# Optimization experiments

Measured on AMD Instinct MI355X. Metric: run time of the kernel, lower is better.

The kernel has to match this reference:

```python
import jax, jax.numpy as jnp
import numpy as np

B, N, F = 4, 3000, 128

def setup_inputs() -> dict:
    key = jax.random.key(0)
    k1, k2, k3, k4 = jax.random.split(key, 4)
    x = jax.random.normal(k1, (B, N, F), dtype=jnp.float32)
    adj = jax.random.uniform(k2, (B, N, N), dtype=jnp.float32)
    h0 = jax.random.normal(k3, (B, N, F), dtype=jnp.float32)
    stdv = 1.0 / np.sqrt(F)
    theta = jax.random.uniform(k4, (F, F), dtype=jnp.float32, minval=-stdv, maxval=stdv)
    return {
        "x": x, "adj": adj, "h0": h0, "theta": theta,
        "lamda": jnp.float32(0.5), "alpha": jnp.float32(0.1), "l": 4,
    }

def _normalize_adj(adj):
    # add self loops, then D^{-1/2} A D^{-1/2} via elementwise row/col scaling
    # (same math as diag-embed + inverse + two bmms in the original)
    n = adj.shape[1]
    adj = adj + jnp.eye(n, dtype=adj.dtype)
    deg = jnp.sum(adj, axis=2)                      # [B, N]
    d_inv_sqrt = jax.lax.rsqrt(deg)                 # [B, N]
    return d_inv_sqrt[:, :, None] * adj * d_inv_sqrt[:, None, :]

def reference(x, adj, h0, theta, lamda, alpha, l):
    adj_n = _normalize_adj(adj)
    beta = jnp.log(lamda / l + 1.0)
    hi = jnp.einsum('bnm,bmf->bnf', adj_n, x)       # aggregation
    support = (1.0 - alpha) * hi + alpha * h0       # variant=False path
    r = support
    out = beta * jnp.einsum('bnf,fg->bng', support, theta) + (1.0 - beta) * r
    return out
```

## Files before the change

kernel.cpp:

```cpp
#include <hip/hip_runtime.h>
#include <hip/hip_bf16.h>
#include <math.h>

#define BB 4
#define NN 3000
#define NR 3008
#define NC 3072
#define FF 128
#define NKC 96
#define NIT 188

typedef __bf16 bf16x8 __attribute__((ext_vector_type(8)));
typedef __bf16 bf16x4 __attribute__((ext_vector_type(4)));
typedef __bf16 bf16x8a __attribute__((ext_vector_type(8), aligned(8)));
typedef __bf16 bf16x4a __attribute__((ext_vector_type(4), aligned(4)));
typedef float  f32x4  __attribute__((ext_vector_type(4)));

__global__ __launch_bounds__(256) void k_degpk2(const float* __restrict__ adj,
                                                float* __restrict__ dis,
                                                __bf16* __restrict__ apk) {
    int wid  = (blockIdx.x * 256 + threadIdx.x) >> 6;
    int lane = threadIdx.x & 63;
    if (wid >= BB * NN) return;
    int b = wid / NN, i = wid - b * NN;
    const float4* row4 = (const float4*)(adj + (size_t)wid * NN);
    __bf16* prow = apk + ((size_t)b * NR + i) * NC;
    float s = 0.f;
    for (int c = lane; c < 768; c += 64) {
        float4 v = {0.f, 0.f, 0.f, 0.f};
        if (c < 750) v = row4[c];
        s += (v.x + v.y) + (v.z + v.w);
        bf16x4a o;
        o[0] = (__bf16)v.x; o[1] = (__bf16)v.y;
        o[2] = (__bf16)v.z; o[3] = (__bf16)v.w;
        *(bf16x4a*)(prow + c * 4) = o;
    }
    for (int off = 32; off > 0; off >>= 1) s += __shfl_down(s, off, 64);
    if (lane == 0) dis[wid] = 1.0f / sqrtf(s + 1.0f);
}

__global__ __launch_bounds__(256) void k_xpk(const float* __restrict__ x,
                                             const float* __restrict__ dis,
                                             const float* __restrict__ theta,
                                             __bf16* __restrict__ xpk,
                                             __bf16* __restrict__ thpk) {
    int b  = blockIdx.y, kc = blockIdx.x;
    int t  = threadIdx.x, w = t >> 6, l = t & 63;
    int m  = l & 15, q = l >> 4;
    #pragma unroll
    for (int h = 0; h < 2; ++h) {
        int nt = w + h * 4;
        int f  = nt * 16 + m;
        bf16x8 v;
        #pragma unroll
        for (int j = 0; j < 8; ++j) {
            int k = kc * 32 + q * 8 + j;
            float val = 0.f;
            if (k < NN) val = dis[b * NN + k] * x[((size_t)b * NN + k) * FF + f];
            v[j] = (__bf16)val;
        }
        *(bf16x8*)(xpk + ((size_t)(b * 8 + nt) * NKC + kc) * 512 + l * 8) = v;
    }
    if (b == 0 && kc < 4) {
        #pragma unroll
        for (int h = 0; h < 2; ++h) {
            int nt = w + h * 4;
            bf16x8 v;
            #pragma unroll
            for (int j = 0; j < 8; ++j) {
                int k = kc * 32 + q * 8 + j;
                v[j] = (__bf16)theta[k * FF + nt * 16 + m];
            }
            *(bf16x8*)(thpk + ((size_t)(nt * 4 + kc)) * 512 + l * 8) = v;
        }
    }
}

__global__ __launch_bounds__(256) void k_aggs2(const __bf16* __restrict__ apk,
                                               const __bf16* __restrict__ xpk,
                                               const __bf16* __restrict__ thpk,
                                               const float* __restrict__ x,
                                               const float* __restrict__ h0,
                                               const float* __restrict__ dis,
                                               float* __restrict__ out,
                                               const float* __restrict__ alpha_p,
                                               const float* __restrict__ lamda_p,
                                               const int* __restrict__ l_p) {
    __shared__ __bf16 stile[16][140];
    const int id = blockIdx.x;
    const int b  = (id >> 1) & 3;
    const int it = (id >> 3) * 2 + (id & 1);
    const int i0 = it * 16;
    const int t  = threadIdx.x, w = t >> 6, l = t & 63;
    const int m  = l & 15, quad = l >> 4;
    const int n0 = w * 32;
    const __bf16* A0 = apk + ((size_t)b * NR + (i0 + m)) * NC + quad * 8;
    const __bf16* B0 = xpk + ((size_t)(b * 8 + 2 * w) * NKC) * 512 + l * 8;
    const __bf16* B1 = B0 + (size_t)NKC * 512;
    f32x4 acc0 = {0.f, 0.f, 0.f, 0.f};
    f32x4 acc1 = {0.f, 0.f, 0.f, 0.f};

    #pragma unroll 8
    for (int kc = 0; kc < NKC; ++kc) {
        bf16x8 a  = *(const bf16x8*)(A0 + kc * 32);
        bf16x8 b0 = *(const bf16x8*)(B0 + (size_t)kc * 512);
        bf16x8 b1 = *(const bf16x8*)(B1 + (size_t)kc * 512);
        acc0 = __builtin_amdgcn_mfma_f32_16x16x32_bf16(a, b0, acc0, 0, 0, 0);
        acc1 = __builtin_amdgcn_mfma_f32_16x16x32_bf16(a, b1, acc1, 0, 0, 0);
    }

    const float alpha = *alpha_p;
    const float beta  = logf(*lamda_p / (float)(*l_p) + 1.0f);
    float s0v[4], s1v[4];
    #pragma unroll
    for (int r = 0; r < 4; ++r) {
        int row  = quad * 4 + r;
        int irow = i0 + row;
        float s0 = 0.f, s1 = 0.f;
        if (irow < NN) {
            float  di   = dis[b * NN + irow];
            size_t base = ((size_t)b * NN + irow) * FF;
            int c0 = n0 + m, c1 = n0 + 16 + m;
            s0 = (1.f - alpha) * (di * acc0[r] + di * di * x[base + c0]) + alpha * h0[base + c0];
            s1 = (1.f - alpha) * (di * acc1[r] + di * di * x[base + c1]) + alpha * h0[base + c1];
        }
        s0v[r] = s0; s1v[r] = s1;
        stile[row][n0 + m]      = (__bf16)s0;
        stile[row][n0 + 16 + m] = (__bf16)s1;
    }
    __syncthreads();
    f32x4 o0 = {0.f, 0.f, 0.f, 0.f};
    f32x4 o1 = {0.f, 0.f, 0.f, 0.f};
    const __bf16* T0 = thpk + (size_t)(2 * w * 4) * 512 + l * 8;
    const __bf16* T1 = T0 + 4 * 512;
    #pragma unroll
    for (int kc = 0; kc < 4; ++kc) {
        bf16x4a alo = *(const bf16x4a*)&stile[m][kc * 32 + quad * 8];
        bf16x4a ahi = *(const bf16x4a*)&stile[m][kc * 32 + quad * 8 + 4];
        bf16x8 a = __builtin_shufflevector(alo, ahi, 0, 1, 2, 3, 4, 5, 6, 7);
        bf16x8 tb0 = *(const bf16x8*)(T0 + (size_t)kc * 512);
        bf16x8 tb1 = *(const bf16x8*)(T1 + (size_t)kc * 512);
        o0 = __builtin_amdgcn_mfma_f32_16x16x32_bf16(a, tb0, o0, 0, 0, 0);
        o1 = __builtin_amdgcn_mfma_f32_16x16x32_bf16(a, tb1, o1, 0, 0, 0);
    }
    const float omb = 1.f - beta;
    #pragma unroll
    for (int r = 0; r < 4; ++r) {
        int irow = i0 + quad * 4 + r;
        if (irow < NN) {
            size_t base = ((size_t)b * NN + irow) * FF;
            out[base + n0 + m]      = beta * o0[r] + omb * s0v[r];
            out[base + n0 + 16 + m] = beta * o1[r] + omb * s1v[r];
        }
    }
}

#define TS 532
__global__ __launch_bounds__(256) void k_deg(const float* __restrict__ adj,
                                             float* __restrict__ dis) {
    int wid  = (blockIdx.x * 256 + threadIdx.x) >> 6;
    int lane = threadIdx.x & 63;
    if (wid >= BB * NN) return;
    const float4* row = (const float4*)(adj + (size_t)wid * NN);
    float s = 0.f;
    for (int c = lane; c < NN / 4; c += 64) {
        float4 v = row[c];
        s += (v.x + v.y) + (v.z + v.w);
    }
    for (int off = 32; off > 0; off >>= 1) s += __shfl_down(s, off, 64);
    if (lane == 0) dis[wid] = 1.0f / sqrtf(s + 1.0f);
}

__global__ __launch_bounds__(256) void k_agg(const float* __restrict__ adj,
                                             const __bf16* __restrict__ xpk,
                                             const __bf16* __restrict__ thpk,
                                             const float* __restrict__ x,
                                             const float* __restrict__ h0,
                                             const float* __restrict__ dis,
                                             float* __restrict__ out,
                                             const float* __restrict__ alpha_p,
                                             const float* __restrict__ lamda_p,
                                             const int* __restrict__ l_p) {
    __shared__ __bf16 tile[2][16][TS];
    __shared__ __bf16 stile[16][140];
    const int id = blockIdx.x;
    const int b  = (id >> 1) & 3;
    const int it = (id >> 3) * 2 + (id & 1);
    const int i0 = it * 16;
    const int t  = threadIdx.x, w = t >> 6, l = t & 63;
    const int m  = l & 15, quad = l >> 4;
    const int n0 = w * 32;
    const __bf16* B0 = xpk + ((size_t)(b * 8 + 2 * w) * NKC) * 512 + l * 8;
    const __bf16* B1 = B0 + (size_t)NKC * 512;
    f32x4 acc0 = {0.f, 0.f, 0.f, 0.f};
    f32x4 acc1 = {0.f, 0.f, 0.f, 0.f};

    float4 pu[4], pv[4];
    auto load_chunk = [&](int c) {
        #pragma unroll
        for (int i = 0; i < 4; ++i) {
            int row  = i * 4 + w;
            int irow = i0 + row;
            int col  = c * 512 + l * 8;
            float4 u = {0.f, 0.f, 0.f, 0.f}, v = {0.f, 0.f, 0.f, 0.f};
            if (irow < NN && col < NN) {
                const float* p = adj + ((size_t)b * NN + irow) * NN + col;
                u = *(const float4*)p;
                v = *(const float4*)(p + 4);
            }
            pu[i] = u; pv[i] = v;
        }
    };
    auto store_chunk = [&](int cb) {
        #pragma unroll
        for (int i = 0; i < 4; ++i) {
            int row = i * 4 + w;
            bf16x8a s;
            s[0] = (__bf16)pu[i].x; s[1] = (__bf16)pu[i].y;
            s[2] = (__bf16)pu[i].z; s[3] = (__bf16)pu[i].w;
            s[4] = (__bf16)pv[i].x; s[5] = (__bf16)pv[i].y;
            s[6] = (__bf16)pv[i].z; s[7] = (__bf16)pv[i].w;
            *(bf16x8a*)&tile[cb][row][l * 8] = s;
        }
    };

    load_chunk(0);
    store_chunk(0);
    __syncthreads();
    for (int c = 0; c < 6; ++c) {
        int cb = c & 1;
        if (c < 5) load_chunk(c + 1);
        #pragma unroll 4
        for (int kcl = 0; kcl < 16; ++kcl) {
            int kc = c * 16 + kcl;
            bf16x8 a = *(const bf16x8a*)&tile[cb][m][kcl * 32 + quad * 8];
            bf16x8 b0 = *(const bf16x8*)(B0 + (size_t)kc * 512);
            bf16x8 b1 = *(const bf16x8*)(B1 + (size_t)kc * 512);
            acc0 = __builtin_amdgcn_mfma_f32_16x16x32_bf16(a, b0, acc0, 0, 0, 0);
            acc1 = __builtin_amdgcn_mfma_f32_16x16x32_bf16(a, b1, acc1, 0, 0, 0);
        }
        if (c < 5) store_chunk(cb ^ 1);
        __syncthreads();
    }

    const float alpha = *alpha_p;
    const float beta  = logf(*lamda_p / (float)(*l_p) + 1.0f);
    float s0v[4], s1v[4];
    #pragma unroll
    for (int r = 0; r < 4; ++r) {
        int row  = quad * 4 + r;
        int irow = i0 + row;
        float s0 = 0.f, s1 = 0.f;
        if (irow < NN) {
            float  di   = dis[b * NN + irow];
            size_t base = ((size_t)b * NN + irow) * FF;
            int c0 = n0 + m, c1 = n0 + 16 + m;
            s0 = (1.f - alpha) * (di * acc0[r] + di * di * x[base + c0]) + alpha * h0[base + c0];
            s1 = (1.f - alpha) * (di * acc1[r] + di * di * x[base + c1]) + alpha * h0[base + c1];
        }
        s0v[r] = s0; s1v[r] = s1;
        stile[row][n0 + m]      = (__bf16)s0;
        stile[row][n0 + 16 + m] = (__bf16)s1;
    }
    __syncthreads();
    f32x4 o0 = {0.f, 0.f, 0.f, 0.f};
    f32x4 o1 = {0.f, 0.f, 0.f, 0.f};
    const __bf16* T0 = thpk + (size_t)(2 * w * 4) * 512 + l * 8;
    const __bf16* T1 = T0 + 4 * 512;
    #pragma unroll
    for (int kc = 0; kc < 4; ++kc) {
        bf16x4a alo = *(const bf16x4a*)&stile[m][kc * 32 + quad * 8];
        bf16x4a ahi = *(const bf16x4a*)&stile[m][kc * 32 + quad * 8 + 4];
        bf16x8 a = __builtin_shufflevector(alo, ahi, 0, 1, 2, 3, 4, 5, 6, 7);
        bf16x8 tb0 = *(const bf16x8*)(T0 + (size_t)kc * 512);
        bf16x8 tb1 = *(const bf16x8*)(T1 + (size_t)kc * 512);
        o0 = __builtin_amdgcn_mfma_f32_16x16x32_bf16(a, tb0, o0, 0, 0, 0);
        o1 = __builtin_amdgcn_mfma_f32_16x16x32_bf16(a, tb1, o1, 0, 0, 0);
    }
    const float omb = 1.f - beta;
    #pragma unroll
    for (int r = 0; r < 4; ++r) {
        int irow = i0 + quad * 4 + r;
        if (irow < NN) {
            size_t base = ((size_t)b * NN + irow) * FF;
            out[base + n0 + m]      = beta * o0[r] + omb * s0v[r];
            out[base + n0 + 16 + m] = beta * o1[r] + omb * s1v[r];
        }
    }
}

__global__ __launch_bounds__(256) void k_thpk_fb(const float* __restrict__ theta,
                                                 __bf16* __restrict__ thpk) {
    int kc = blockIdx.x;
    int t  = threadIdx.x, w = t >> 6, l = t & 63;
    int m  = l & 15, q = l >> 4;
    #pragma unroll
    for (int h = 0; h < 2; ++h) {
        int nt = w + h * 4;
        bf16x8 v;
        #pragma unroll
        for (int j = 0; j < 8; ++j) {
            int k = kc * 32 + q * 8 + j;
            v[j] = (__bf16)theta[k * FF + nt * 16 + m];
        }
        *(bf16x8*)(thpk + ((size_t)(nt * 4 + kc)) * 512 + l * 8) = v;
    }
}

__global__ __launch_bounds__(256) void k_xpk_fb(const float* __restrict__ x,
                                                const float* __restrict__ dis,
                                                __bf16* __restrict__ xpk) {
    int b  = blockIdx.y, kc = blockIdx.x;
    int t  = threadIdx.x, w = t >> 6, l = t & 63;
    int m  = l & 15, q = l >> 4;
    #pragma unroll
    for (int h = 0; h < 2; ++h) {
        int nt = w + h * 4;
        int f  = nt * 16 + m;
        bf16x8 v;
        #pragma unroll
        for (int j = 0; j < 8; ++j) {
            int k = kc * 32 + q * 8 + j;
            float val = 0.f;
            if (k < NN) val = dis[b * NN + k] * x[((size_t)b * NN + k) * FF + f];
            v[j] = (__bf16)val;
        }
        *(bf16x8*)(xpk + ((size_t)(b * 8 + nt) * NKC + kc) * 512 + l * 8) = v;
    }
}


extern "C" void kernel_launch(void* const* d_in, const int* in_sizes, int n_in,
                              void* d_out, int out_size, void* d_ws, size_t ws_size,
                              hipStream_t stream) {
    const float* x      = (const float*)d_in[0];
    const float* adj    = (const float*)d_in[1];
    const float* h0     = (const float*)d_in[2];
    const float* theta  = (const float*)d_in[3];
    const float* lamda  = (const float*)d_in[4];
    const float* alpha  = (const float*)d_in[5];
    const int*   l      = (const int*)d_in[6];
    float* out = (float*)d_out;

    char* ws = (char*)d_ws;

    const size_t APK_OFF = 3276800;
    const size_t WS_NEED = APK_OFF + (size_t)BB * NR * NC * 2;

    if (ws_size >= WS_NEED) {
        float*  dis  = (float*)ws;
        __bf16* thpk = (__bf16*)(ws + 65536);
        __bf16* xpk  = (__bf16*)(ws + 131072);
        __bf16* apk  = (__bf16*)(ws + APK_OFF);

        k_degpk2<<<dim3((BB * NN) / 4), 256, 0, stream>>>(adj, dis, apk);
        k_xpk<<<dim3(NKC, BB), 256, 0, stream>>>(x, dis, theta, xpk, thpk);
        k_aggs2<<<dim3(NIT * BB), 256, 0, stream>>>(apk, xpk, thpk, x, h0, dis, out,
                                                    alpha, lamda, l);
    } else {
        float*  dis  = (float*)ws;
        __bf16* xpk  = (__bf16*)(ws + 65536);
        __bf16* thpk = (__bf16*)(ws + 3276800);

        k_deg<<<dim3((BB * NN) / 4), 256, 0, stream>>>(adj, dis);
        k_thpk_fb<<<dim3(4), 256, 0, stream>>>(theta, thpk);
        k_xpk_fb<<<dim3(NKC, BB), 256, 0, stream>>>(x, dis, xpk);
        k_agg<<<dim3(NIT * BB), 256, 0, stream>>>(adj, xpk, thpk, x, h0, dis, out,
                                                  alpha, lamda, l);
    }
}
```

Measured before the change: 305.6 us.

## Stage packed adjacency rows through double-buffered LDS in aggregation kernel

The aggregation kernel now loads 512-column chunks of the packed bf16 adjacency with coalesced row-wide loads into a double-buffered shared tile. It prefetches the next chunk into registers while MFMAs consume the current one. Previously each lane read strided 16-byte pieces directly from global memory. The packing kernel also now covers the padding rows (NR instead of NN) and writes zeros there, so the padded tile rows are defined. The cost is extra LDS traffic, more shared memory per block and a barrier per chunk.

```diff
diff --git a/kernel.cpp b/kernel.cpp
--- a/kernel.cpp
+++ b/kernel.cpp
@@ -9,6 +9,7 @@
 #define FF 128
 #define NKC 96
 #define NIT 188
+#define TS  532
 
 typedef __bf16 bf16x8 __attribute__((ext_vector_type(8)));
 typedef __bf16 bf16x4 __attribute__((ext_vector_type(4)));
@@ -21,14 +22,15 @@
                                                 __bf16* __restrict__ apk) {
     int wid  = (blockIdx.x * 256 + threadIdx.x) >> 6;
     int lane = threadIdx.x & 63;
-    if (wid >= BB * NN) return;
-    int b = wid / NN, i = wid - b * NN;
-    const float4* row4 = (const float4*)(adj + (size_t)wid * NN);
+    if (wid >= BB * NR) return;
+    int b = wid / NR, i = wid - b * NR;
+    const bool rowv = i < NN;
+    const float4* row4 = (const float4*)(adj + ((size_t)b * NN + i) * NN);
     __bf16* prow = apk + ((size_t)b * NR + i) * NC;
     float s = 0.f;
     for (int c = lane; c < 768; c += 64) {
         float4 v = {0.f, 0.f, 0.f, 0.f};
-        if (c < 750) v = row4[c];
+        if (rowv && c < 750) v = row4[c];
         s += (v.x + v.y) + (v.z + v.w);
         bf16x4a o;
         o[0] = (__bf16)v.x; o[1] = (__bf16)v.y;
@@ -36,7 +38,7 @@
         *(bf16x4a*)(prow + c * 4) = o;
     }
     for (int off = 32; off > 0; off >>= 1) s += __shfl_down(s, off, 64);
-    if (lane == 0) dis[wid] = 1.0f / sqrtf(s + 1.0f);
+    if (lane == 0 && rowv) dis[b * NN + i] = 1.0f / sqrtf(s + 1.0f);
 }
 
 __global__ __launch_bounds__(256) void k_xpk(const float* __restrict__ x,
@@ -76,16 +78,17 @@
     }
 }
 
-__global__ __launch_bounds__(256) void k_aggs2(const __bf16* __restrict__ apk,
-                                               const __bf16* __restrict__ xpk,
-                                               const __bf16* __restrict__ thpk,
-                                               const float* __restrict__ x,
-                                               const float* __restrict__ h0,
-                                               const float* __restrict__ dis,
-                                               float* __restrict__ out,
-                                               const float* __restrict__ alpha_p,
-                                               const float* __restrict__ lamda_p,
-                                               const int* __restrict__ l_p) {
+__global__ __launch_bounds__(256) void k_agg3(const __bf16* __restrict__ apk,
+                                              const __bf16* __restrict__ xpk,
+                                              const __bf16* __restrict__ thpk,
+                                              const float* __restrict__ x,
+                                              const float* __restrict__ h0,
+                                              const float* __restrict__ dis,
+                                              float* __restrict__ out,
+                                              const float* __restrict__ alpha_p,
+                                              const float* __restrict__ lamda_p,
+                                              const int* __restrict__ l_p) {
+    __shared__ __bf16 tile[2][16][TS];
     __shared__ __bf16 stile[16][140];
     const int id = blockIdx.x;
     const int b  = (id >> 1) & 3;
@@ -94,19 +97,45 @@
     const int t  = threadIdx.x, w = t >> 6, l = t & 63;
     const int m  = l & 15, quad = l >> 4;
     const int n0 = w * 32;
-    const __bf16* A0 = apk + ((size_t)b * NR + (i0 + m)) * NC + quad * 8;
+    const __bf16* Abase = apk + ((size_t)b * NR + i0) * NC;
     const __bf16* B0 = xpk + ((size_t)(b * 8 + 2 * w) * NKC) * 512 + l * 8;
     const __bf16* B1 = B0 + (size_t)NKC * 512;
     f32x4 acc0 = {0.f, 0.f, 0.f, 0.f};
     f32x4 acc1 = {0.f, 0.f, 0.f, 0.f};
 
-    #pragma unroll 8
-    for (int kc = 0; kc < NKC; ++kc) {
-        bf16x8 a  = *(const bf16x8*)(A0 + kc * 32);
-        bf16x8 b0 = *(const bf16x8*)(B0 + (size_t)kc * 512);
-        bf16x8 b1 = *(const bf16x8*)(B1 + (size_t)kc * 512);
-        acc0 = __builtin_amdgcn_mfma_f32_16x16x32_bf16(a, b0, acc0, 0, 0, 0);
-        acc1 = __builtin_amdgcn_mfma_f32_16x16x32_bf16(a, b1, acc1, 0, 0, 0);
+    bf16x8a st[4];
+    auto load_chunk = [&](int c) {
+        #pragma unroll
+        for (int i = 0; i < 4; ++i) {
+            int row = i * 4 + w;
+            st[i] = *(const bf16x8a*)(Abase + (size_t)row * NC + c * 512 + l * 8);
+        }
+    };
+    auto store_chunk = [&](int cb) {
+        #pragma unroll
+        for (int i = 0; i < 4; ++i) {
+            int row = i * 4 + w;
+            *(bf16x8a*)&tile[cb][row][l * 8] = st[i];
+        }
+    };
+
+    load_chunk(0);
+    store_chunk(0);
+    __syncthreads();
+    for (int c = 0; c < 6; ++c) {
+        int cb = c & 1;
+        if (c < 5) load_chunk(c + 1);
+        #pragma unroll 4
+        for (int kcl = 0; kcl < 16; ++kcl) {
+            int kc = c * 16 + kcl;
+            bf16x8 a = *(const bf16x8a*)&tile[cb][m][kcl * 32 + quad * 8];
+            bf16x8 b0 = *(const bf16x8*)(B0 + (size_t)kc * 512);
+            bf16x8 b1 = *(const bf16x8*)(B1 + (size_t)kc * 512);
+            acc0 = __builtin_amdgcn_mfma_f32_16x16x32_bf16(a, b0, acc0, 0, 0, 0);
+            acc1 = __builtin_amdgcn_mfma_f32_16x16x32_bf16(a, b1, acc1, 0, 0, 0);
+        }
+        if (c < 5) store_chunk(cb ^ 1);
+        __syncthreads();
     }
 
     const float alpha = *alpha_p;
@@ -155,7 +184,6 @@
     }
 }
 
-#define TS 532
 __global__ __launch_bounds__(256) void k_deg(const float* __restrict__ adj,
                                              float* __restrict__ dis) {
     int wid  = (blockIdx.x * 256 + threadIdx.x) >> 6;
@@ -353,10 +381,10 @@
         __bf16* xpk  = (__bf16*)(ws + 131072);
         __bf16* apk  = (__bf16*)(ws + APK_OFF);
 
-        k_degpk2<<<dim3((BB * NN) / 4), 256, 0, stream>>>(adj, dis, apk);
+        k_degpk2<<<dim3((BB * NR) / 4), 256, 0, stream>>>(adj, dis, apk);
         k_xpk<<<dim3(NKC, BB), 256, 0, stream>>>(x, dis, theta, xpk, thpk);
-        k_aggs2<<<dim3(NIT * BB), 256, 0, stream>>>(apk, xpk, thpk, x, h0, dis, out,
-                                                    alpha, lamda, l);
+        k_agg3<<<dim3(NIT * BB), 256, 0, stream>>>(apk, xpk, thpk, x, h0, dis, out,
+                                                   alpha, lamda, l);
     } else {
         float*  dis  = (float*)ws;
         __bf16* xpk  = (__bf16*)(ws + 65536);
```

Result: faster. 281.2 us (-8.0%).
